# Performance work log

Hardware: AMD Instinct MI355X
Metric: run time of the kernel (lower is better)

## Reference

```python
import jax, jax.numpy as jnp
import numpy as np

NUM_NODES = 100000
NUM_EDGES = 3200000
NUM_GRAPHS = 64


def gcn_conv(x, edge_index, W, b):
    """PyG GCNConv: add self-loops, symmetric deg normalization, linear, scatter-add."""
    n = x.shape[0]
    loop = jnp.arange(n, dtype=edge_index.dtype)
    src = jnp.concatenate([edge_index[0], loop])  # message sources
    dst = jnp.concatenate([edge_index[1], loop])  # aggregation targets
    deg = jax.ops.segment_sum(jnp.ones_like(src, dtype=x.dtype), dst, num_segments=n)
    dis = jnp.where(deg > 0, jax.lax.rsqrt(jnp.maximum(deg, 1.0)), 0.0)
    norm = dis[src] * dis[dst]  # [E+N]
    h = x @ W  # linear transform first (small dims)
    msg = h[src] * norm[:, None]  # irregular gather
    out = jax.ops.segment_sum(msg, dst, num_segments=n)  # scatter-add
    return out + b


def setup_inputs() -> dict:
    key = jax.random.key(0)
    ks = jax.random.split(key, 12)
    x = jax.random.normal(ks[0], (NUM_NODES, 3), dtype=jnp.float32)
    edge_index = jax.random.randint(ks[1], (2, NUM_EDGES), 0, NUM_NODES, dtype=jnp.int64)
    batch = jnp.sort(jax.random.randint(ks[2], (NUM_NODES,), 0, NUM_GRAPHS, dtype=jnp.int64))
    def glorot(k, fan_in, fan_out):
        s = (6.0 / (fan_in + fan_out)) ** 0.5
        return jax.random.uniform(k, (fan_in, fan_out), jnp.float32, -s, s)
    return {
        'x': x, 'edge_index': edge_index, 'batch': batch,
        'W1': glorot(ks[3], 3, 32), 'b1': jnp.zeros((32,), jnp.float32),
        'W2': glorot(ks[4], 32, 16), 'b2': jnp.zeros((16,), jnp.float32),
        'W3': glorot(ks[5], 16, 8), 'b3': jnp.zeros((8,), jnp.float32),
        'Wf': glorot(ks[6], 8, 3), 'bf': jnp.zeros((3,), jnp.float32),
    }


def reference(x, edge_index, batch, W1, b1, W2, b2, W3, b3, Wf, bf):
    h = jax.nn.relu(gcn_conv(x, edge_index, W1, b1))
    h = jax.nn.relu(gcn_conv(h, edge_index, W2, b2))
    h = jax.nn.relu(gcn_conv(h, edge_index, W3, b3))
    # global mean pool over graphs
    sums = jax.ops.segment_sum(h, batch, num_segments=NUM_GRAPHS)
    cnts = jax.ops.segment_sum(jnp.ones((h.shape[0],), h.dtype), batch, num_segments=NUM_GRAPHS)
    pooled = sums / jnp.maximum(cnts, 1.0)[:, None]
    return pooled @ Wf + bf
```

## Files before the change

kernel.cpp:

```cpp
#include <hip/hip_runtime.h>

constexpr int N_NODES  = 100000;
constexpr int N_EDGES  = 3200000;
constexpr int N_GRAPHS = 64;

constexpr int BSHIFT   = 8;
constexpr int NBINS    = (N_NODES + 255) >> BSHIFT;
constexpr int BIN_CAP  = 9216;
constexpr int SRC_BITS = 17;
constexpr int SRC_MASK = (1 << SRC_BITS) - 1;

constexpr int NB_BIN = 500;
constexpr int EPB    = N_EDGES / NB_BIN;
constexpr int EPT    = (EPB + 1023) / 1024;

typedef float v4f __attribute__((ext_vector_type(4)));


__global__ __launch_bounds__(1024) void bin_kernel(
        const int* __restrict__ src, const int* __restrict__ dst,
        int* __restrict__ bin_cur, int* __restrict__ binned) {
    __shared__ int pk[EPB];
    __shared__ unsigned short bn[EPB];
    __shared__ unsigned short ord[EPB];
    __shared__ int hist[NBINS];
    __shared__ int lexcl[NBINS];
    __shared__ int lofs[NBINS];
    __shared__ int gofs[NBINS];
    __shared__ int s512[512];
    int tid = threadIdx.x;
    int e0 = blockIdx.x * EPB;
    for (int i = tid; i < NBINS; i += 1024) hist[i] = 0;
    __syncthreads();
#pragma unroll
    for (int k = 0; k < EPT; ++k) {
        int i = tid + k * 1024;
        if (i < EPB) {
            int d = __builtin_nontemporal_load(&dst[e0 + i]);
            int s = __builtin_nontemporal_load(&src[e0 + i]);
            int b = d >> BSHIFT;
            pk[i] = ((d & 255) << SRC_BITS) | s;
            bn[i] = (unsigned short)b;
            atomicAdd(&hist[b], 1);
        }
    }
    __syncthreads();
    if (tid < 512) s512[tid] = (tid < NBINS) ? hist[tid] : 0;
    __syncthreads();
    for (int o = 1; o < 512; o <<= 1) {
        int x = 0;
        if (tid < 512 && tid >= o) x = s512[tid - o];
        __syncthreads();
        if (tid < 512) s512[tid] += x;
        __syncthreads();
    }
    if (tid < NBINS) {
        int h = hist[tid];
        int excl = s512[tid] - h;
        lexcl[tid] = excl;
        lofs[tid]  = excl;
        gofs[tid]  = h ? atomicAdd(&bin_cur[tid], h) : 0;
    }
    __syncthreads();
#pragma unroll
    for (int k = 0; k < EPT; ++k) {
        int i = tid + k * 1024;
        if (i < EPB) {
            int r = atomicAdd(&lofs[bn[i]], 1);
            ord[r] = (unsigned short)i;
        }
    }
    __syncthreads();
#pragma unroll
    for (int k = 0; k < EPT; ++k) {
        int i = tid + k * 1024;
        if (i < EPB) {
            int j = ord[i];
            int b = bn[j];
            int pos = gofs[b] + (i - lexcl[b]);
            if (pos < BIN_CAP)
                __builtin_nontemporal_store(pk[j], &binned[(size_t)b * BIN_CAP + pos]);
        }
    }
}

__global__ void binscan_kernel(const int* __restrict__ bin_cur, int* __restrict__ bin_base,
                               int* __restrict__ rowptr) {
    __shared__ int s[512];
    int t = threadIdx.x;
    int v = (t < NBINS) ? bin_cur[t] : 0;
    s[t] = v;
    __syncthreads();
    for (int o = 1; o < 512; o <<= 1) {
        int x = (t >= o) ? s[t - o] : 0;
        __syncthreads();
        s[t] += x;
        __syncthreads();
    }
    if (t < NBINS) bin_base[t] = s[t] - v;
    if (t == 0) rowptr[N_NODES] = N_EDGES;
}

__global__ __launch_bounds__(1024) void csrbuild_kernel(
        const int* __restrict__ binned, const int* __restrict__ bin_cur,
        const int* __restrict__ bin_base, int* __restrict__ rowptr,
        float* __restrict__ dis, int* __restrict__ csr) {
    __shared__ int cnt[256];
    __shared__ int lofs[256];
    __shared__ int s[256];
    int b = blockIdx.x;
    int t = threadIdx.x;
    int size  = min(bin_cur[b], BIN_CAP);
    int gbase = bin_base[b];
    const int* bp = binned + (size_t)b * BIN_CAP;
    if (t < 256) cnt[t] = 0;
    __syncthreads();
    int pc[9];
#pragma unroll
    for (int k = 0; k < 9; ++k) {
        int i = t + k * 1024;
        pc[k] = (i < size) ? __builtin_nontemporal_load(&bp[i]) : -1;
        if (i < size) atomicAdd(&cnt[pc[k] >> SRC_BITS], 1);
    }
    __syncthreads();
    if (t < 256) {
        int n = (b << BSHIFT) + t;
        int deg = cnt[t];
        if (n < N_NODES) dis[n] = 1.0f / sqrtf((float)deg + 1.0f);
        s[t] = deg;
    }
    __syncthreads();
    for (int o = 1; o < 256; o <<= 1) {
        int x = 0;
        if (t < 256 && t >= o) x = s[t - o];
        __syncthreads();
        if (t < 256) s[t] += x;
        __syncthreads();
    }
    if (t < 256) {
        int n = (b << BSHIFT) + t;
        int excl = s[t] - cnt[t];
        if (n < N_NODES) rowptr[n] = gbase + excl;
        lofs[t] = excl;
        cnt[t] = 0;
    }
    __syncthreads();
#pragma unroll
    for (int k = 0; k < 9; ++k) {
        int i = t + k * 1024;
        if (i < size) {
            int p = pc[k];
            int ln = p >> SRC_BITS;
            int r = atomicAdd(&cnt[ln], 1);
            csr[gbase + lofs[ln] + r] = p & SRC_MASK;
        }
    }
}


__global__ void pre1_kernel(const float* __restrict__ x, const float* __restrict__ dis,
                            float* __restrict__ xs) {
    int i = blockIdx.x * blockDim.x + threadIdx.x;
    if (i >= N_NODES) return;
    float d = dis[i];
    float4 v;
    v.x = __builtin_nontemporal_load(&x[(size_t)i * 3 + 0]) * d;
    v.y = __builtin_nontemporal_load(&x[(size_t)i * 3 + 1]) * d;
    v.z = __builtin_nontemporal_load(&x[(size_t)i * 3 + 2]) * d;
    v.w = 0.f;
    *reinterpret_cast<float4*>(&xs[(size_t)i * 4]) = v;
}

template<int F, bool ADD_B, bool RELU>
__global__ __launch_bounds__(256) void gather_kernel(
        const float* __restrict__ in, const int* __restrict__ rowptr,
        const int* __restrict__ csr, const float* __restrict__ dis,
        const float* __restrict__ b, float* __restrict__ out) {
    constexpr int VPL = F / 4;
    constexpr int NPB = 256 / 16;
    int tid  = threadIdx.x;
    int sub  = tid & 3;
    int qtr  = (tid >> 2) & 3;
    int n    = blockIdx.x * NPB + (tid >> 4);
    if (n >= N_NODES) return;
    int beg = rowptr[n], end = rowptr[n + 1];
    int len = end - beg;
    int kb = beg + ((len * qtr) >> 2);
    int ke = beg + ((len * (qtr + 1)) >> 2);
    const float* ip = in + (size_t)sub * VPL;
    float a0[VPL], a1[VPL], a2[VPL], a3[VPL];
#pragma unroll
    for (int j = 0; j < VPL; ++j) { a0[j] = 0.f; a1[j] = 0.f; a2[j] = 0.f; a3[j] = 0.f; }
    if (qtr == 0) {
#pragma unroll
        for (int j = 0; j < VPL; ++j) a0[j] = ip[(size_t)n * F + j];
    }
    int k = kb;
    for (; k + 7 < ke; k += 8) {
        int s0 = __builtin_nontemporal_load(&csr[k + 0]);
        int s1 = __builtin_nontemporal_load(&csr[k + 1]);
        int s2 = __builtin_nontemporal_load(&csr[k + 2]);
        int s3 = __builtin_nontemporal_load(&csr[k + 3]);
        int s4 = __builtin_nontemporal_load(&csr[k + 4]);
        int s5 = __builtin_nontemporal_load(&csr[k + 5]);
        int s6 = __builtin_nontemporal_load(&csr[k + 6]);
        int s7 = __builtin_nontemporal_load(&csr[k + 7]);
        const float* r0 = &ip[(size_t)s0 * F];
        const float* r1 = &ip[(size_t)s1 * F];
        const float* r2 = &ip[(size_t)s2 * F];
        const float* r3 = &ip[(size_t)s3 * F];
        const float* r4 = &ip[(size_t)s4 * F];
        const float* r5 = &ip[(size_t)s5 * F];
        const float* r6 = &ip[(size_t)s6 * F];
        const float* r7 = &ip[(size_t)s7 * F];
#pragma unroll
        for (int j = 0; j < VPL; ++j) a0[j] += r0[j];
#pragma unroll
        for (int j = 0; j < VPL; ++j) a1[j] += r1[j];
#pragma unroll
        for (int j = 0; j < VPL; ++j) a2[j] += r2[j];
#pragma unroll
        for (int j = 0; j < VPL; ++j) a3[j] += r3[j];
#pragma unroll
        for (int j = 0; j < VPL; ++j) a0[j] += r4[j];
#pragma unroll
        for (int j = 0; j < VPL; ++j) a1[j] += r5[j];
#pragma unroll
        for (int j = 0; j < VPL; ++j) a2[j] += r6[j];
#pragma unroll
        for (int j = 0; j < VPL; ++j) a3[j] += r7[j];
    }
    if (k + 3 < ke) {
        int s0 = __builtin_nontemporal_load(&csr[k + 0]);
        int s1 = __builtin_nontemporal_load(&csr[k + 1]);
        int s2 = __builtin_nontemporal_load(&csr[k + 2]);
        int s3 = __builtin_nontemporal_load(&csr[k + 3]);
        const float* r0 = &ip[(size_t)s0 * F];
        const float* r1 = &ip[(size_t)s1 * F];
        const float* r2 = &ip[(size_t)s2 * F];
        const float* r3 = &ip[(size_t)s3 * F];
#pragma unroll
        for (int j = 0; j < VPL; ++j) a0[j] += r0[j];
#pragma unroll
        for (int j = 0; j < VPL; ++j) a1[j] += r1[j];
#pragma unroll
        for (int j = 0; j < VPL; ++j) a2[j] += r2[j];
#pragma unroll
        for (int j = 0; j < VPL; ++j) a3[j] += r3[j];
        k += 4;
    }
    for (; k < ke; ++k) {
        int s0 = __builtin_nontemporal_load(&csr[k]);
        const float* r0 = &ip[(size_t)s0 * F];
#pragma unroll
        for (int j = 0; j < VPL; ++j) a0[j] += r0[j];
    }
    float v[VPL];
#pragma unroll
    for (int j = 0; j < VPL; ++j) v[j] = (a0[j] + a1[j]) + (a2[j] + a3[j]);
#pragma unroll
    for (int j = 0; j < VPL; ++j) v[j] += __shfl_xor(v[j], 4);
#pragma unroll
    for (int j = 0; j < VPL; ++j) v[j] += __shfl_xor(v[j], 8);
    if (qtr == 0) {
        float d = dis[n];
#pragma unroll
        for (int j = 0; j < VPL; ++j) {
            float w = v[j] * d;
            if (ADD_B) w += b[sub * VPL + j];
            if (RELU) w = fmaxf(w, 0.f);
            __builtin_nontemporal_store(w, &out[(size_t)n * F + sub * VPL + j]);
        }
    }
}

__global__ __launch_bounds__(256) void gather16w3_kernel(
        const float* __restrict__ in, const int* __restrict__ rowptr,
        const int* __restrict__ csr, const float* __restrict__ dis,
        const float* __restrict__ b2, const float* __restrict__ W3,
        float* __restrict__ g8) {
    __shared__ float w3s[128];
    int tid = threadIdx.x;
    if (tid < 128) w3s[tid] = W3[tid];
    __syncthreads();
    constexpr int F = 16, VPL = 4;
    int sub = tid & 3, qtr = (tid >> 2) & 3;
    int n = blockIdx.x * 16 + (tid >> 4);
    int beg = rowptr[n], end = rowptr[n + 1];
    int len = end - beg;
    int kb = beg + ((len * qtr) >> 2);
    int ke = beg + ((len * (qtr + 1)) >> 2);
    const float* ip = in + (size_t)sub * VPL;
    float a0[4], a1[4], a2[4], a3[4];
#pragma unroll
    for (int j = 0; j < 4; ++j) { a1[j] = 0.f; a2[j] = 0.f; a3[j] = 0.f; }
#pragma unroll
    for (int j = 0; j < 4; ++j) a0[j] = (qtr == 0) ? ip[(size_t)n * F + j] : 0.f;
    int k = kb;
    for (; k + 7 < ke; k += 8) {
        int s0 = __builtin_nontemporal_load(&csr[k + 0]);
        int s1 = __builtin_nontemporal_load(&csr[k + 1]);
        int s2 = __builtin_nontemporal_load(&csr[k + 2]);
        int s3 = __builtin_nontemporal_load(&csr[k + 3]);
        int s4 = __builtin_nontemporal_load(&csr[k + 4]);
        int s5 = __builtin_nontemporal_load(&csr[k + 5]);
        int s6 = __builtin_nontemporal_load(&csr[k + 6]);
        int s7 = __builtin_nontemporal_load(&csr[k + 7]);
        const float* r0 = &ip[(size_t)s0 * F];
        const float* r1 = &ip[(size_t)s1 * F];
        const float* r2 = &ip[(size_t)s2 * F];
        const float* r3 = &ip[(size_t)s3 * F];
        const float* r4 = &ip[(size_t)s4 * F];
        const float* r5 = &ip[(size_t)s5 * F];
        const float* r6 = &ip[(size_t)s6 * F];
        const float* r7 = &ip[(size_t)s7 * F];
#pragma unroll
        for (int j = 0; j < 4; ++j) a0[j] += r0[j];
#pragma unroll
        for (int j = 0; j < 4; ++j) a1[j] += r1[j];
#pragma unroll
        for (int j = 0; j < 4; ++j) a2[j] += r2[j];
#pragma unroll
        for (int j = 0; j < 4; ++j) a3[j] += r3[j];
#pragma unroll
        for (int j = 0; j < 4; ++j) a0[j] += r4[j];
#pragma unroll
        for (int j = 0; j < 4; ++j) a1[j] += r5[j];
#pragma unroll
        for (int j = 0; j < 4; ++j) a2[j] += r6[j];
#pragma unroll
        for (int j = 0; j < 4; ++j) a3[j] += r7[j];
    }
    if (k + 3 < ke) {
        int s0 = __builtin_nontemporal_load(&csr[k + 0]);
        int s1 = __builtin_nontemporal_load(&csr[k + 1]);
        int s2 = __builtin_nontemporal_load(&csr[k + 2]);
        int s3 = __builtin_nontemporal_load(&csr[k + 3]);
        const float* r0 = &ip[(size_t)s0 * F];
        const float* r1 = &ip[(size_t)s1 * F];
        const float* r2 = &ip[(size_t)s2 * F];
        const float* r3 = &ip[(size_t)s3 * F];
#pragma unroll
        for (int j = 0; j < 4; ++j) a0[j] += r0[j];
#pragma unroll
        for (int j = 0; j < 4; ++j) a1[j] += r1[j];
#pragma unroll
        for (int j = 0; j < 4; ++j) a2[j] += r2[j];
#pragma unroll
        for (int j = 0; j < 4; ++j) a3[j] += r3[j];
        k += 4;
    }
    for (; k < ke; ++k) {
        int s0 = __builtin_nontemporal_load(&csr[k]);
        const float* r0 = &ip[(size_t)s0 * F];
#pragma unroll
        for (int j = 0; j < 4; ++j) a0[j] += r0[j];
    }
    float d = dis[n];
    float w[4];
#pragma unroll
    for (int j = 0; j < 4; ++j) {
        float v = (a0[j] + a1[j]) + (a2[j] + a3[j]);
        v += __shfl_xor(v, 4);
        v += __shfl_xor(v, 8);
        w[j] = fmaxf(fmaf(v, d, b2[sub * 4 + j]), 0.f);
    }
    float p[8];
#pragma unroll
    for (int o = 0; o < 8; ++o) {
        float s = 0.f;
#pragma unroll
        for (int j = 0; j < 4; ++j) s = fmaf(w[j], w3s[(sub * 4 + j) * 8 + o], s);
        s += __shfl_xor(s, 1);
        s += __shfl_xor(s, 2);
        p[o] = s;
    }
    if (qtr == 0) {
        __builtin_nontemporal_store(p[sub * 2 + 0] * d, &g8[(size_t)n * 8 + sub * 2 + 0]);
        __builtin_nontemporal_store(p[sub * 2 + 1] * d, &g8[(size_t)n * 8 + sub * 2 + 1]);
    }
}

__global__ __launch_bounds__(256) void linfuse_kernel(
        const float* __restrict__ m, const float* __restrict__ W1,
        const float* __restrict__ b1, const float* __restrict__ W2,
        const float* __restrict__ dis, float* __restrict__ g) {
    __shared__ float w2s[512];
    __shared__ float w1s[96];
    __shared__ float b1s[32];
    int tid = threadIdx.x;
    for (int j = tid; j < 512; j += 256) w2s[j] = W2[j];
    if (tid < 96) w1s[tid] = W1[tid];
    if (tid < 32) b1s[tid] = b1[tid];
    __syncthreads();
    int i = blockIdx.x * blockDim.x + tid;
    if (i >= N_NODES) return;
    float4 mv = *reinterpret_cast<const float4*>(&m[(size_t)i * 4]);
    float h[32];
#pragma unroll
    for (int f = 0; f < 32; ++f) {
        float s = b1s[f];
        s = fmaf(mv.x, w1s[f], s);
        s = fmaf(mv.y, w1s[32 + f], s);
        s = fmaf(mv.z, w1s[64 + f], s);
        h[f] = fmaxf(s, 0.f);
    }
    float d = dis[i];
#pragma unroll
    for (int o = 0; o < 16; ++o) {
        float s = 0.f;
#pragma unroll
        for (int f = 0; f < 32; ++f) s = fmaf(h[f], w2s[f * 16 + o], s);
        g[(size_t)i * 16 + o] = s * d;
    }
}


__global__ void pool_kernel(const float* __restrict__ h, const int* __restrict__ batch,
                            float* __restrict__ pool) {
    __shared__ float lsum[N_GRAPHS * 8];
    __shared__ float lcnt[N_GRAPHS];
    int tid = threadIdx.x;
    for (int j = tid; j < N_GRAPHS * 8; j += blockDim.x) lsum[j] = 0.f;
    for (int j = tid; j < N_GRAPHS; j += blockDim.x) lcnt[j] = 0.f;
    __syncthreads();
    int i = blockIdx.x * blockDim.x + tid;
    if (i < N_NODES) {
        int gm = batch[i];
        const float4* hp = reinterpret_cast<const float4*>(&h[(size_t)i * 8]);
        float4 a = hp[0], bq = hp[1];
        atomicAdd(&lsum[gm * 8 + 0], a.x);
        atomicAdd(&lsum[gm * 8 + 1], a.y);
        atomicAdd(&lsum[gm * 8 + 2], a.z);
        atomicAdd(&lsum[gm * 8 + 3], a.w);
        atomicAdd(&lsum[gm * 8 + 4], bq.x);
        atomicAdd(&lsum[gm * 8 + 5], bq.y);
        atomicAdd(&lsum[gm * 8 + 6], bq.z);
        atomicAdd(&lsum[gm * 8 + 7], bq.w);
        atomicAdd(&lcnt[gm], 1.0f);
    }
    __syncthreads();
    for (int idx = tid; idx < N_GRAPHS * 9; idx += blockDim.x) {
        int gm = idx / 9, j = idx % 9;
        if (lcnt[gm] != 0.f) {
            if (j < 8) atomicAdd(&pool[gm * 8 + j], lsum[gm * 8 + j]);
            else       atomicAdd(&pool[512 + gm], lcnt[gm]);
        }
    }
}

__global__ void final_kernel(const float* __restrict__ pool, const float* __restrict__ Wf,
                             const float* __restrict__ bf, float* __restrict__ out) {
    int t = threadIdx.x;
    if (t >= N_GRAPHS * 3) return;
    int gm = t / 3, c = t % 3;
    float cnt = fmaxf(pool[512 + gm], 1.0f);
    float s = 0.f;
#pragma unroll
    for (int f = 0; f < 8; ++f) s = fmaf(pool[gm * 8 + f] / cnt, Wf[f * 3 + c], s);
    out[t] = s + bf[c];
}


extern "C" void kernel_launch(void* const* d_in, const int* in_sizes, int n_in,
                              void* d_out, int out_size, void* d_ws, size_t ws_size,
                              hipStream_t stream) {
    const float* x     = (const float*)d_in[0];
    const int*   ei    = (const int*)d_in[1];
    const int*   batch = (const int*)d_in[2];
    const float* W1 = (const float*)d_in[3];
    const float* b1 = (const float*)d_in[4];
    const float* W2 = (const float*)d_in[5];
    const float* b2 = (const float*)d_in[6];
    const float* W3 = (const float*)d_in[7];
    const float* b3 = (const float*)d_in[8];
    const float* Wf = (const float*)d_in[9];
    const float* bf = (const float*)d_in[10];

    const int* src = ei;
    const int* dst = ei + N_EDGES;

    const int N = N_NODES;

    int*   bin_cur  = (int*)d_ws;
    int*   bin_base = bin_cur + NBINS;
    int*   rowptr   = bin_base + NBINS;
    float* dis      = (float*)(rowptr + N + 2);
    int*   csr      = (int*)(dis + N);
    float* act      = (float*)(csr + N_EDGES);
    int*   binned   = (int*)act;
    float* xs   = act;
    float* m    = act + (size_t)4  * N;
    float* g    = act + (size_t)8  * N;
    float* g8   = act + (size_t)24 * N;
    float* h3   = act;
    float* pool = act + (size_t)36 * N;

    const int B = 256;
    const int NB_N = (N + B - 1) / B;
    const int NB_G = N / 16;

    hipMemsetAsync(bin_cur, 0, NBINS * sizeof(int), stream);
    hipMemsetAsync(pool, 0, N_GRAPHS * 9 * sizeof(float), stream);

    bin_kernel<<<NB_BIN, 1024, 0, stream>>>(src, dst, bin_cur, binned);
    binscan_kernel<<<1, 512, 0, stream>>>(bin_cur, bin_base, rowptr);
    csrbuild_kernel<<<NBINS, 1024, 0, stream>>>(binned, bin_cur, bin_base, rowptr, dis, csr);

    pre1_kernel<<<NB_N, B, 0, stream>>>(x, dis, xs);
    gather_kernel<4, false, false><<<NB_G, B, 0, stream>>>(xs, rowptr, csr, dis, b1, m);
    linfuse_kernel<<<NB_N, B, 0, stream>>>(m, W1, b1, W2, dis, g);

    gather16w3_kernel<<<NB_G, B, 0, stream>>>(g, rowptr, csr, dis, b2, W3, g8);

    gather_kernel<8, true, true><<<NB_G, B, 0, stream>>>(g8, rowptr, csr, dis, b3, h3);

    pool_kernel<<<NB_N, B, 0, stream>>>(h3, batch, pool);
    final_kernel<<<1, 256, 0, stream>>>(pool, Wf, bf, (float*)d_out);
}
```

Before: 183.8 us.

## Fuse pre-scaling into CSR build, reuse first-pass ranks, transpose W3, shrink pool grid

The separate pre1 kernel is removed: the CSR build now computes the scaled input features right after it computes node degrees. The local rank returned by the first shared-memory atomic is stored per element and reused, so the second atomic pass is gone. W3 is stored transposed in shared memory, which changes the bank access pattern, and the pool kernel uses a 64-block grid-stride loop to cut the number of global atomics. The costs are that the scaled features are written into a separately placed buffer, and the pool kernel has less parallelism.

```diff
diff --git a/kernel.cpp b/kernel.cpp
--- a/kernel.cpp
+++ b/kernel.cpp
@@ -103,8 +103,9 @@
 
 __global__ __launch_bounds__(1024) void csrbuild_kernel(
         const int* __restrict__ binned, const int* __restrict__ bin_cur,
-        const int* __restrict__ bin_base, int* __restrict__ rowptr,
-        float* __restrict__ dis, int* __restrict__ csr) {
+        const int* __restrict__ bin_base, const float* __restrict__ x,
+        int* __restrict__ rowptr, float* __restrict__ dis,
+        float* __restrict__ xs, int* __restrict__ csr) {
     __shared__ int cnt[256];
     __shared__ int lofs[256];
     __shared__ int s[256];
@@ -116,25 +117,38 @@
     if (t < 256) cnt[t] = 0;
     __syncthreads();
     int pc[9];
+    unsigned char rk[9];
 #pragma unroll
     for (int k = 0; k < 9; ++k) {
         int i = t + k * 1024;
-        pc[k] = (i < size) ? __builtin_nontemporal_load(&bp[i]) : -1;
-        if (i < size) atomicAdd(&cnt[pc[k] >> SRC_BITS], 1);
+        pc[k] = -1; rk[k] = 0;
+        if (i < size) {
+            pc[k] = __builtin_nontemporal_load(&bp[i]);
+            rk[k] = (unsigned char)atomicAdd(&cnt[pc[k] >> SRC_BITS], 1);
+        }
     }
     __syncthreads();
     if (t < 256) {
         int n = (b << BSHIFT) + t;
         int deg = cnt[t];
-        if (n < N_NODES) dis[n] = 1.0f / sqrtf((float)deg + 1.0f);
+        if (n < N_NODES) {
+            float di = 1.0f / sqrtf((float)deg + 1.0f);
+            dis[n] = di;
+            float4 v;
+            v.x = __builtin_nontemporal_load(&x[(size_t)n * 3 + 0]) * di;
+            v.y = __builtin_nontemporal_load(&x[(size_t)n * 3 + 1]) * di;
+            v.z = __builtin_nontemporal_load(&x[(size_t)n * 3 + 2]) * di;
+            v.w = 0.f;
+            *reinterpret_cast<float4*>(&xs[(size_t)n * 4]) = v;
+        }
         s[t] = deg;
     }
     __syncthreads();
     for (int o = 1; o < 256; o <<= 1) {
-        int x = 0;
-        if (t < 256 && t >= o) x = s[t - o];
+        int xum = 0;
+        if (t < 256 && t >= o) xum = s[t - o];
         __syncthreads();
-        if (t < 256) s[t] += x;
+        if (t < 256) s[t] += xum;
         __syncthreads();
     }
     if (t < 256) {
@@ -142,7 +156,6 @@
         int excl = s[t] - cnt[t];
         if (n < N_NODES) rowptr[n] = gbase + excl;
         lofs[t] = excl;
-        cnt[t] = 0;
     }
     __syncthreads();
 #pragma unroll
@@ -151,25 +164,11 @@
         if (i < size) {
             int p = pc[k];
             int ln = p >> SRC_BITS;
-            int r = atomicAdd(&cnt[ln], 1);
-            csr[gbase + lofs[ln] + r] = p & SRC_MASK;
-        }
-    }
-}
-
-
-__global__ void pre1_kernel(const float* __restrict__ x, const float* __restrict__ dis,
-                            float* __restrict__ xs) {
-    int i = blockIdx.x * blockDim.x + threadIdx.x;
-    if (i >= N_NODES) return;
-    float d = dis[i];
-    float4 v;
-    v.x = __builtin_nontemporal_load(&x[(size_t)i * 3 + 0]) * d;
-    v.y = __builtin_nontemporal_load(&x[(size_t)i * 3 + 1]) * d;
-    v.z = __builtin_nontemporal_load(&x[(size_t)i * 3 + 2]) * d;
-    v.w = 0.f;
-    *reinterpret_cast<float4*>(&xs[(size_t)i * 4]) = v;
-}
+            csr[gbase + lofs[ln] + rk[k]] = p & SRC_MASK;
+        }
+    }
+}
+
 
 template<int F, bool ADD_B, bool RELU>
 __global__ __launch_bounds__(256) void gather_kernel(
@@ -281,7 +280,10 @@
         float* __restrict__ g8) {
     __shared__ float w3s[128];
     int tid = threadIdx.x;
-    if (tid < 128) w3s[tid] = W3[tid];
+    if (tid < 128) {
+        int f = tid >> 3, o = tid & 7;
+        w3s[o * 16 + f] = W3[tid];
+    }
     __syncthreads();
     constexpr int F = 16, VPL = 4;
     int sub = tid & 3, qtr = (tid >> 2) & 3;
@@ -370,7 +372,7 @@
     for (int o = 0; o < 8; ++o) {
         float s = 0.f;
 #pragma unroll
-        for (int j = 0; j < 4; ++j) s = fmaf(w[j], w3s[(sub * 4 + j) * 8 + o], s);
+        for (int j = 0; j < 4; ++j) s = fmaf(w[j], w3s[o * 16 + sub * 4 + j], s);
         s += __shfl_xor(s, 1);
         s += __shfl_xor(s, 2);
         p[o] = s;
@@ -416,16 +418,16 @@
 }
 
 
-__global__ void pool_kernel(const float* __restrict__ h, const int* __restrict__ batch,
-                            float* __restrict__ pool) {
+__global__ __launch_bounds__(256) void pool_kernel(
+        const float* __restrict__ h, const int* __restrict__ batch,
+        float* __restrict__ pool) {
     __shared__ float lsum[N_GRAPHS * 8];
     __shared__ float lcnt[N_GRAPHS];
     int tid = threadIdx.x;
-    for (int j = tid; j < N_GRAPHS * 8; j += blockDim.x) lsum[j] = 0.f;
-    for (int j = tid; j < N_GRAPHS; j += blockDim.x) lcnt[j] = 0.f;
-    __syncthreads();
-    int i = blockIdx.x * blockDim.x + tid;
-    if (i < N_NODES) {
+    for (int j = tid; j < N_GRAPHS * 8; j += 256) lsum[j] = 0.f;
+    if (tid < N_GRAPHS) lcnt[tid] = 0.f;
+    __syncthreads();
+    for (int i = blockIdx.x * 256 + tid; i < N_NODES; i += gridDim.x * 256) {
         int gm = batch[i];
         const float4* hp = reinterpret_cast<const float4*>(&h[(size_t)i * 8]);
         float4 a = hp[0], bq = hp[1];
@@ -440,7 +442,7 @@
         atomicAdd(&lcnt[gm], 1.0f);
     }
     __syncthreads();
-    for (int idx = tid; idx < N_GRAPHS * 9; idx += blockDim.x) {
+    for (int idx = tid; idx < N_GRAPHS * 9; idx += 256) {
         int gm = idx / 9, j = idx % 9;
         if (lcnt[gm] != 0.f) {
             if (j < 8) atomicAdd(&pool[gm * 8 + j], lsum[gm * 8 + j]);
@@ -489,12 +491,12 @@
     int*   csr      = (int*)(dis + N);
     float* act      = (float*)(csr + N_EDGES);
     int*   binned   = (int*)act;
-    float* xs   = act;
     float* m    = act + (size_t)4  * N;
     float* g    = act + (size_t)8  * N;
     float* g8   = act + (size_t)24 * N;
+    float* xs   = act + (size_t)36 * N;
     float* h3   = act;
-    float* pool = act + (size_t)36 * N;
+    float* pool = act + (size_t)40 * N;
 
     const int B = 256;
     const int NB_N = (N + B - 1) / B;
@@ -505,9 +507,9 @@
 
     bin_kernel<<<NB_BIN, 1024, 0, stream>>>(src, dst, bin_cur, binned);
     binscan_kernel<<<1, 512, 0, stream>>>(bin_cur, bin_base, rowptr);
-    csrbuild_kernel<<<NBINS, 1024, 0, stream>>>(binned, bin_cur, bin_base, rowptr, dis, csr);
-
-    pre1_kernel<<<NB_N, B, 0, stream>>>(x, dis, xs);
+    csrbuild_kernel<<<NBINS, 1024, 0, stream>>>(binned, bin_cur, bin_base, x,
+                                                rowptr, dis, xs, csr);
+
     gather_kernel<4, false, false><<<NB_G, B, 0, stream>>>(xs, rowptr, csr, dis, b1, m);
     linfuse_kernel<<<NB_N, B, 0, stream>>>(m, W1, b1, W2, dis, g);
 
@@ -515,6 +517,6 @@
 
     gather_kernel<8, true, true><<<NB_G, B, 0, stream>>>(g8, rowptr, csr, dis, b3, h3);
 
-    pool_kernel<<<NB_N, B, 0, stream>>>(h3, batch, pool);
+    pool_kernel<<<64, B, 0, stream>>>(h3, batch, pool);
     final_kernel<<<1, 256, 0, stream>>>(pool, Wf, bf, (float*)d_out);
 }
```

New measurement: 202.5 us. 1.1x slower.
